# Performance work log

Hardware: AMD Instinct MI355X
Metric: run time of the kernel (lower is better)

The kernel has to match this reference:

```python
import jax, jax.numpy as jnp
import numpy as np

D = 128
EPS = 1e-6


def setup_inputs() -> dict:
    key = jax.random.key(0)
    k1, k2, k3, k4 = jax.random.split(key, 4)
    N, NQ, NK = 32, 2048, 2048
    queries = jax.random.normal(k1, (N, NQ, D), dtype=jnp.float32)
    keys = jax.random.normal(k2, (N, NK, D), dtype=jnp.float32)
    values = jax.random.normal(k3, (N, NK, D), dtype=jnp.float32)
    # multiplicative (soft) mask in [0,1)
    mask = jax.random.uniform(k4, (N, NQ, NK), dtype=jnp.float32)
    return {"queries": queries, "keys": keys, "values": values, "mask": mask}


def reference(queries, keys, values, mask):
    # scaled dot-product scores: N x n_q x n_k
    scaled = jnp.einsum("bqd,bkd->bqk", queries, keys) / jnp.sqrt(jnp.float32(D))
    attn = jax.nn.softmax(scaled, axis=2)
    # post-softmax multiplicative masking + renormalization
    attn = attn * mask
    attn = attn / (jnp.sum(attn, axis=2, keepdims=True) + EPS)
    return jnp.einsum("bqk,bkd->bqd", attn, values)
```

## Files before the change

kernel.cpp:

```cpp
#include <hip/hip_runtime.h>

#define NB   32
#define NQL  2048
#define NKL  2048
#define DH   128
#define QBLK 64
#define KBLK 64
#define NT   (NKL / KBLK)
#define EPS  1e-6f

typedef __bf16 bf16x8 __attribute__((ext_vector_type(8)));
typedef __bf16 bf16x4 __attribute__((ext_vector_type(4)));
typedef float  f32x4  __attribute__((ext_vector_type(4)));

__global__ __launch_bounds__(256) void
prep_k(const float* __restrict__ Kg, unsigned short* __restrict__ Kimg)
{
    const int blk = blockIdx.x;
    const int t   = threadIdx.x;
    const int rK  = t >> 2;
    const int x0  = (t & 3) * 32;
    const int swz = (rK & 7) << 3;
    const float* src = Kg + ((size_t)blk * 64 + rK) * DH;
    unsigned short* dst = Kimg + ((size_t)blk << 13) + rK * 128;
    #pragma unroll
    for (int i = 0; i < 4; ++i) {
        const int c0 = (x0 + i * 8) ^ swz;
        float4 a = *(const float4*)(src + c0);
        float4 c = *(const float4*)(src + c0 + 4);
        *(bf16x8*)(dst + x0 + i * 8) =
            (bf16x8){ (__bf16)a.x, (__bf16)a.y, (__bf16)a.z, (__bf16)a.w,
                      (__bf16)c.x, (__bf16)c.y, (__bf16)c.z, (__bf16)c.w };
    }
}

__global__ __launch_bounds__(256) void
prep_v(const float* __restrict__ Vg, unsigned short* __restrict__ Vimg)
{
    __shared__ float T[64 * 132];
    const int blk = blockIdx.x;
    const int t   = threadIdx.x;
    {
        const int r  = t >> 2;
        const int c0 = (t & 3) * 32;
        const float* src = Vg + ((size_t)blk * 64 + r) * DH + c0;
        #pragma unroll
        for (int j = 0; j < 8; ++j)
            *(float4*)&T[r * 132 + c0 + j * 4] = *(const float4*)(src + j * 4);
    }
    __syncthreads();
    {
        const int dV  = t >> 1;
        const int yh  = (t & 1) * 32;
        const int swz = (dV & 7) << 3;
        unsigned short* dst = Vimg + ((size_t)blk << 13) + dV * 64 + yh;
        #pragma unroll
        for (int i = 0; i < 4; ++i) {
            const int ks = (yh + i * 8) ^ swz;
            bf16x8 o;
            #pragma unroll
            for (int j = 0; j < 8; ++j) o[j] = (__bf16)T[(ks + j) * 132 + dV];
            *(bf16x8*)(dst + i * 8) = o;
        }
    }
}

#define GLL16(GSRC, LDST) \
    __builtin_amdgcn_global_load_lds( \
        (const __attribute__((address_space(1))) void*)(GSRC), \
        (__attribute__((address_space(3))) void*)(LDST), 16, 0, 0)

#define ISSUE_KV(KT, KB, VB) do { \
    const size_t tb_ = ((size_t)(b * 32 + (KT))) << 14;                \
    const char* ksrc_ = (const char*)KimgB + tb_ + woff + lby;                    \
    const char* vsrc_ = (const char*)VimgB + tb_ + woff + lby;                    \
    char* kd_ = (char*)(KB) + woff;                                               \
    char* vd_ = (char*)(VB) + woff;                                               \
    GLL16(ksrc_ +    0, kd_ +    0);  GLL16(ksrc_ + 1024, kd_ + 1024);            \
    GLL16(ksrc_ + 2048, kd_ + 2048);  GLL16(ksrc_ + 3072, kd_ + 3072);            \
    GLL16(vsrc_ +    0, vd_ +    0);  GLL16(vsrc_ + 1024, vd_ + 1024);            \
    GLL16(vsrc_ + 2048, vd_ + 2048);  GLL16(vsrc_ + 3072, vd_ + 3072);            \
} while (0)

#define LOAD_M(K0, R0, R1, R2, R3) do { \
    const float* mb_ = mbase + (K0) + lg * 4; \
    R0 = *(const float4*)(mb_ +  0);  R1 = *(const float4*)(mb_ + 16); \
    R2 = *(const float4*)(mb_ + 32);  R3 = *(const float4*)(mb_ + 48); \
} while (0)

#define COMPUTE(KB, VB, M0, M1, M2, M3) do { \
    f32x4 sacc[4]; \
    _Pragma("unroll") for (int m = 0; m < 4; ++m) sacc[m] = (f32x4){0.f,0.f,0.f,0.f}; \
    __builtin_amdgcn_s_setprio(1); \
    _Pragma("unroll") for (int m = 0; m < 4; ++m) { \
        _Pragma("unroll") for (int c = 0; c < 4; ++c) { \
            bf16x8 af = *(bf16x8*)&KB[(m * 16 + lq) * 128 + ((c * 32 + lg * 8) ^ swzL)]; \
            sacc[m] = __builtin_amdgcn_mfma_f32_16x16x32_bf16(af, qf[c], sacc[m], 0, 0, 0); \
        } \
    } \
    __builtin_amdgcn_s_setprio(0); \
    float mk_[16] = { M0.x, M0.y, M0.z, M0.w,  M1.x, M1.y, M1.z, M1.w, \
                      M2.x, M2.y, M2.z, M2.w,  M3.x, M3.y, M3.z, M3.w }; \
    float sv[4][4], tmax = -1e30f; \
    _Pragma("unroll") for (int m = 0; m < 4; ++m) \
        _Pragma("unroll") for (int r = 0; r < 4; ++r) { \
            sv[m][r] = sacc[m][r] * scale; \
            tmax = fmaxf(tmax, sv[m][r]); \
        } \
    tmax = fmaxf(tmax, __shfl_xor(tmax, 16)); \
    tmax = fmaxf(tmax, __shfl_xor(tmax, 32)); \
    if (!__all(tmax - m_run <= 8.f)) { \
        const float mnew  = fmaxf(m_run, tmax); \
        const float alpha = __expf(m_run - mnew); \
        m_run = mnew;  z_part *= alpha;  s_part *= alpha; \
        float alr[4]; \
        _Pragma("unroll") for (int r = 0; r < 4; ++r) alr[r] = __shfl(alpha, lg * 4 + r); \
        _Pragma("unroll") for (int n = 0; n < 8; ++n) \
            _Pragma("unroll") for (int r = 0; r < 4; ++r) oacc[n][r] *= alr[r]; \
    } \
    float zl = 0.f, sl = 0.f, pm[4][4]; \
    _Pragma("unroll") for (int m = 0; m < 4; ++m) \
        _Pragma("unroll") for (int r = 0; r < 4; ++r) { \
            float p = __expf(sv[m][r] - m_run); \
            zl += p; \
            float pq = p * mk_[m * 4 + r]; \
            sl += pq;  pm[m][r] = pq; \
        } \
    z_part += zl;  s_part += sl; \
    _Pragma("unroll") for (int m = 0; m < 4; ++m) \
        *(bf16x4*)&Ps[w][lq][m * 16 + lg * 4] = \
            (bf16x4){ (__bf16)pm[m][0], (__bf16)pm[m][1], (__bf16)pm[m][2], (__bf16)pm[m][3] }; \
    __builtin_amdgcn_s_setprio(1); \
    _Pragma("unroll") for (int kc = 0; kc < 2; ++kc) { \
        bf16x8 pa = *(bf16x8*)&Ps[w][lq][kc * 32 + lg * 8]; \
        _Pragma("unroll") for (int n = 0; n < 8; ++n) { \
            bf16x8 vv = *(bf16x8*)&VB[(n * 16 + lq) * 64 + ((kc * 32 + lg * 8) ^ swzL)]; \
            oacc[n] = __builtin_amdgcn_mfma_f32_16x16x32_bf16(pa, vv, oacc[n], 0, 0, 0); \
        } \
    } \
    __builtin_amdgcn_s_setprio(0); \
} while (0)

#define ITER(KT, KBc, VBc, KBn, VBn, MU0,MU1,MU2,MU3, ML0,ML1,ML2,ML3, LAST) do { \
    if (!(LAST)) { \
        ISSUE_KV((KT) + 1, KBn, VBn); \
        LOAD_M(((KT) + 1) * KBLK, ML0, ML1, ML2, ML3); \
    } \
    __builtin_amdgcn_sched_barrier(0); \
    COMPUTE(KBc, VBc, MU0, MU1, MU2, MU3); \
    if (!(LAST)) __syncthreads(); \
} while (0)

__global__ __launch_bounds__(256, 2) void
attn_main(const float* __restrict__ Qg, const unsigned short* __restrict__ Kimg,
          const unsigned short* __restrict__ Vimg, const float* __restrict__ Mg,
          float* __restrict__ Og)
{
    const int wg = ((blockIdx.x & 7) << 7) | (blockIdx.x >> 3);
    const int b  = wg >> 5;
    const int q0 = (wg & 31) * QBLK;

    const int t  = threadIdx.x;
    const int w  = t >> 6;
    const int l  = t & 63;
    const int lq = l & 15;
    const int lg = l >> 4;
    const int swzL = (lq & 7) << 3;
    const int woff = w * 4096;
    const int lby  = l * 16;

    __shared__ __align__(16) unsigned short Kb0[64 * 128];
    __shared__ __align__(16) unsigned short Kb1[64 * 128];
    __shared__ __align__(16) unsigned short Vb0[128 * 64];
    __shared__ __align__(16) unsigned short Vb1[128 * 64];
    __shared__ __align__(16) unsigned short Ps[4][16][72];

    const char* KimgB = (const char*)Kimg;
    const char* VimgB = (const char*)Vimg;

    const int qrow = q0 + w * 16 + lq;

    bf16x8 qf[4];
    {
        const float* qb = Qg + ((size_t)b * NQL + qrow) * DH;
        #pragma unroll
        for (int c = 0; c < 4; ++c) {
            const float* p = qb + c * 32 + lg * 8;
            float4 x = *(const float4*)(p);
            float4 y = *(const float4*)(p + 4);
            qf[c] = (bf16x8){ (__bf16)x.x, (__bf16)x.y, (__bf16)x.z, (__bf16)x.w,
                              (__bf16)y.x, (__bf16)y.y, (__bf16)y.z, (__bf16)y.w };
        }
    }

    float m_run = -1e30f, z_part = 0.f, s_part = 0.f;
    f32x4 oacc[8];
    #pragma unroll
    for (int n = 0; n < 8; ++n) oacc[n] = (f32x4){0.f, 0.f, 0.f, 0.f};

    const float* mbase = Mg + ((size_t)b * NQL + qrow) * NKL;
    const float scale = 0.08838834764831845f;

    float4 mA0, mA1, mA2, mA3, mB0, mB1, mB2, mB3;

    ISSUE_KV(0, Kb0, Vb0);
    LOAD_M(0, mA0, mA1, mA2, mA3);
    __syncthreads();

    for (int kt = 0; kt < NT - 2; kt += 2) {
        ITER(kt,     Kb0, Vb0, Kb1, Vb1, mA0,mA1,mA2,mA3, mB0,mB1,mB2,mB3, 0);
        ITER(kt + 1, Kb1, Vb1, Kb0, Vb0, mB0,mB1,mB2,mB3, mA0,mA1,mA2,mA3, 0);
    }
    ITER(NT - 2, Kb0, Vb0, Kb1, Vb1, mA0,mA1,mA2,mA3, mB0,mB1,mB2,mB3, 0);
    ITER(NT - 1, Kb1, Vb1, Kb0, Vb0, mB0,mB1,mB2,mB3, mA0,mA1,mA2,mA3, 1);

    float z = z_part + __shfl_xor(z_part, 16);
    z += __shfl_xor(z, 32);
    float s = s_part + __shfl_xor(s_part, 16);
    s += __shfl_xor(s, 32);
    const float inv = 1.f / (s + EPS * z);
    float ivr[4];
    #pragma unroll
    for (int r = 0; r < 4; ++r) ivr[r] = __shfl(inv, lg * 4 + r);

    float* ob = Og + ((size_t)b * NQL + q0 + w * 16) * DH;
    #pragma unroll
    for (int n = 0; n < 8; ++n)
        #pragma unroll
        for (int r = 0; r < 4; ++r)
            ob[(size_t)(lg * 4 + r) * DH + n * 16 + lq] = oacc[n][r] * ivr[r];
}

__global__ __launch_bounds__(256, 3) void
attn_fb(const float* __restrict__ Qg, const float* __restrict__ Kg,
        const float* __restrict__ Vg, const float* __restrict__ Mg,
        float* __restrict__ Og)
{
    const int wg = ((blockIdx.x & 7) << 7) | (blockIdx.x >> 3);
    const int b  = wg >> 5;
    const int q0 = (wg & 31) * QBLK;
    const int t  = threadIdx.x;
    const int w  = t >> 6;
    const int l  = t & 63;
    const int lq = l & 15;
    const int lg = l >> 4;
    __shared__ __align__(16) unsigned short Ks[64 * 128];
    __shared__ __align__(16) unsigned short Vs[128 * 64];
    __shared__ __align__(16) unsigned short Ps[4][16][72];
    const int rK   = t >> 2;
    const int cK   = (t & 3) * 32;
    const int dV   = t >> 1;
    const int khV  = t & 1;
    const int swzK = (rK & 7) << 3;
    const int swzV = (dV & 7) << 3;
    const int swzL = (lq & 7) << 3;
    const int qrow = q0 + w * 16 + lq;
    bf16x8 qf[4];
    {
        const float* qb = Qg + ((size_t)b * NQL + qrow) * DH;
        #pragma unroll
        for (int c = 0; c < 4; ++c) {
            const float* p = qb + c * 32 + lg * 8;
            float4 x = *(const float4*)(p);
            float4 y = *(const float4*)(p + 4);
            qf[c] = (bf16x8){ (__bf16)x.x, (__bf16)x.y, (__bf16)x.z, (__bf16)x.w,
                              (__bf16)y.x, (__bf16)y.y, (__bf16)y.z, (__bf16)y.w };
        }
    }
    float m_run = -1e30f, z_part = 0.f, s_part = 0.f;
    f32x4 oacc[8];
    #pragma unroll
    for (int n = 0; n < 8; ++n) oacc[n] = (f32x4){0.f, 0.f, 0.f, 0.f};
    const float* kbase = Kg + (size_t)b * NKL * DH;
    const float* vbase = Vg + (size_t)b * NKL * DH;
    const float* mbase = Mg + ((size_t)b * NQL + qrow) * NKL;
    const float scale = 0.08838834764831845f;
    for (int kt = 0; kt < NT; ++kt) {
        const int k0 = kt * KBLK;
        float mkf[16];
        {
            const float* mb = mbase + k0 + lg * 4;
            #pragma unroll
            for (int m = 0; m < 4; ++m) {
                float4 x = *(const float4*)(mb + m * 16);
                mkf[m*4+0]=x.x; mkf[m*4+1]=x.y; mkf[m*4+2]=x.z; mkf[m*4+3]=x.w;
            }
        }
        __syncthreads();
        {
            const float* kb = kbase + (size_t)(k0 + rK) * DH + cK;
            #pragma unroll
            for (int i = 0; i < 4; ++i) {
                float4 a = *(const float4*)(kb + i * 8);
                float4 c = *(const float4*)(kb + i * 8 + 4);
                *(bf16x8*)&Ks[rK * 128 + ((cK + i * 8) ^ swzK)] =
                    (bf16x8){ (__bf16)a.x, (__bf16)a.y, (__bf16)a.z, (__bf16)a.w,
                              (__bf16)c.x, (__bf16)c.y, (__bf16)c.z, (__bf16)c.w };
            }
            const float* vb = vbase + (size_t)(k0 + khV * 32) * DH + dV;
            #pragma unroll
            for (int i = 0; i < 4; ++i) {
                bf16x8 o;
                #pragma unroll
                for (int j = 0; j < 8; ++j) o[j] = (__bf16)vb[(i * 8 + j) * DH];
                *(bf16x8*)&Vs[dV * 64 + (((khV << 5) + i * 8) ^ swzV)] = o;
            }
        }
        __syncthreads();
        f32x4 sacc[4];
        #pragma unroll
        for (int m = 0; m < 4; ++m) sacc[m] = (f32x4){0.f,0.f,0.f,0.f};
        #pragma unroll
        for (int m = 0; m < 4; ++m)
            #pragma unroll
            for (int c = 0; c < 4; ++c) {
                bf16x8 af = *(bf16x8*)&Ks[(m * 16 + lq) * 128 + ((c * 32 + lg * 8) ^ swzL)];
                sacc[m] = __builtin_amdgcn_mfma_f32_16x16x32_bf16(af, qf[c], sacc[m], 0, 0, 0);
            }
        float sv[4][4], tmax = -1e30f;
        #pragma unroll
        for (int m = 0; m < 4; ++m)
            #pragma unroll
            for (int r = 0; r < 4; ++r) {
                sv[m][r] = sacc[m][r] * scale;
                tmax = fmaxf(tmax, sv[m][r]);
            }
        tmax = fmaxf(tmax, __shfl_xor(tmax, 16));
        tmax = fmaxf(tmax, __shfl_xor(tmax, 32));
        if (!__all(tmax - m_run <= 8.f)) {
            const float mnew  = fmaxf(m_run, tmax);
            const float alpha = __expf(m_run - mnew);
            m_run = mnew; z_part *= alpha; s_part *= alpha;
            float alr[4];
            #pragma unroll
            for (int r = 0; r < 4; ++r) alr[r] = __shfl(alpha, lg * 4 + r);
            #pragma unroll
            for (int n = 0; n < 8; ++n)
                #pragma unroll
                for (int r = 0; r < 4; ++r) oacc[n][r] *= alr[r];
        }
        float zl = 0.f, sl = 0.f, pm[4][4];
        #pragma unroll
        for (int m = 0; m < 4; ++m)
            #pragma unroll
            for (int r = 0; r < 4; ++r) {
                float p = __expf(sv[m][r] - m_run);
                zl += p;
                float pq = p * mkf[m * 4 + r];
                sl += pq; pm[m][r] = pq;
            }
        z_part += zl; s_part += sl;
        #pragma unroll
        for (int m = 0; m < 4; ++m)
            *(bf16x4*)&Ps[w][lq][m * 16 + lg * 4] =
                (bf16x4){ (__bf16)pm[m][0], (__bf16)pm[m][1], (__bf16)pm[m][2], (__bf16)pm[m][3] };
        #pragma unroll
        for (int kc = 0; kc < 2; ++kc) {
            bf16x8 pa = *(bf16x8*)&Ps[w][lq][kc * 32 + lg * 8];
            #pragma unroll
            for (int n = 0; n < 8; ++n) {
                bf16x8 vv = *(bf16x8*)&Vs[(n * 16 + lq) * 64 + ((kc * 32 + lg * 8) ^ swzL)];
                oacc[n] = __builtin_amdgcn_mfma_f32_16x16x32_bf16(pa, vv, oacc[n], 0, 0, 0);
            }
        }
    }
    float z = z_part + __shfl_xor(z_part, 16);
    z += __shfl_xor(z, 32);
    float s = s_part + __shfl_xor(s_part, 16);
    s += __shfl_xor(s, 32);
    const float inv = 1.f / (s + EPS * z);
    float ivr[4];
    #pragma unroll
    for (int r = 0; r < 4; ++r) ivr[r] = __shfl(inv, lg * 4 + r);
    float* ob = Og + ((size_t)b * NQL + q0 + w * 16) * DH;
    #pragma unroll
    for (int n = 0; n < 8; ++n)
        #pragma unroll
        for (int r = 0; r < 4; ++r)
            ob[(size_t)(lg * 4 + r) * DH + n * 16 + lq] = oacc[n][r] * ivr[r];
}

extern "C" void kernel_launch(void* const* d_in, const int* in_sizes, int n_in,
                              void* d_out, int out_size, void* d_ws, size_t ws_size,
                              hipStream_t stream)
{
    (void)in_sizes; (void)n_in; (void)out_size;
    const float* Q = (const float*)d_in[0];
    const float* K = (const float*)d_in[1];
    const float* V = (const float*)d_in[2];
    const float* M = (const float*)d_in[3];
    float* O = (float*)d_out;

    const size_t imgElems = (size_t)NB * NKL * DH;
    const size_t need     = 2 * imgElems * sizeof(unsigned short);

    if (ws_size >= need) {
        unsigned short* Kimg = (unsigned short*)d_ws;
        unsigned short* Vimg = Kimg + imgElems;
        prep_k<<<dim3(NB * NT), 256, 0, stream>>>(K, Kimg);
        prep_v<<<dim3(NB * NT), 256, 0, stream>>>(V, Vimg);
        attn_main<<<dim3(NB * (NQL / QBLK)), 256, 0, stream>>>(Q, Kimg, Vimg, M, O);
    } else {
        attn_fb<<<dim3(NB * (NQL / QBLK)), 256, 0, stream>>>(Q, K, V, M, O);
    }
}
```

Baseline: 195.3 us.

## Stage K/V tiles through registers two tiles ahead and merge prep kernels

Replaces the direct global-to-LDS async loads with register-staged loads that fetch tile kt+2 into VGPRs while tile kt computes, then write them to LDS at the start of the next iteration. The full __syncthreads is replaced by an lgkmcnt wait plus s_barrier, so outstanding global loads (the prefetched tile and mask) no longer have to drain at each barrier. The K and V prep kernels are merged into a single launch. The cost is extra VGPR pressure under launch_bounds(256,2) and extra LDS write instructions. The code relies on KimgB/VimgB being char pointers, which is set up in lines not shown.

```diff
diff --git a/kernel.cpp b/kernel.cpp
--- a/kernel.cpp
+++ b/kernel.cpp
@@ -14,72 +14,72 @@
 typedef float  f32x4  __attribute__((ext_vector_type(4)));
 
 __global__ __launch_bounds__(256) void
-prep_k(const float* __restrict__ Kg, unsigned short* __restrict__ Kimg)
-{
-    const int blk = blockIdx.x;
-    const int t   = threadIdx.x;
-    const int rK  = t >> 2;
-    const int x0  = (t & 3) * 32;
-    const int swz = (rK & 7) << 3;
-    const float* src = Kg + ((size_t)blk * 64 + rK) * DH;
-    unsigned short* dst = Kimg + ((size_t)blk << 13) + rK * 128;
-    #pragma unroll
-    for (int i = 0; i < 4; ++i) {
-        const int c0 = (x0 + i * 8) ^ swz;
-        float4 a = *(const float4*)(src + c0);
-        float4 c = *(const float4*)(src + c0 + 4);
-        *(bf16x8*)(dst + x0 + i * 8) =
-            (bf16x8){ (__bf16)a.x, (__bf16)a.y, (__bf16)a.z, (__bf16)a.w,
-                      (__bf16)c.x, (__bf16)c.y, (__bf16)c.z, (__bf16)c.w };
-    }
-}
-
-__global__ __launch_bounds__(256) void
-prep_v(const float* __restrict__ Vg, unsigned short* __restrict__ Vimg)
+prep_kv(const float* __restrict__ Kg, const float* __restrict__ Vg,
+        unsigned short* __restrict__ Kimg, unsigned short* __restrict__ Vimg)
 {
     __shared__ float T[64 * 132];
-    const int blk = blockIdx.x;
-    const int t   = threadIdx.x;
-    {
-        const int r  = t >> 2;
-        const int c0 = (t & 3) * 32;
-        const float* src = Vg + ((size_t)blk * 64 + r) * DH + c0;
-        #pragma unroll
-        for (int j = 0; j < 8; ++j)
-            *(float4*)&T[r * 132 + c0 + j * 4] = *(const float4*)(src + j * 4);
-    }
-    __syncthreads();
-    {
-        const int dV  = t >> 1;
-        const int yh  = (t & 1) * 32;
-        const int swz = (dV & 7) << 3;
-        unsigned short* dst = Vimg + ((size_t)blk << 13) + dV * 64 + yh;
+    const int t = threadIdx.x;
+    if (blockIdx.x < NB * NT) {
+        const int blk = blockIdx.x;
+        const int rK  = t >> 2;
+        const int x0  = (t & 3) * 32;
+        const int swz = (rK & 7) << 3;
+        const float* src = Kg + ((size_t)blk * 64 + rK) * DH;
+        unsigned short* dst = Kimg + ((size_t)blk << 13) + rK * 128;
         #pragma unroll
         for (int i = 0; i < 4; ++i) {
-            const int ks = (yh + i * 8) ^ swz;
-            bf16x8 o;
-            #pragma unroll
-            for (int j = 0; j < 8; ++j) o[j] = (__bf16)T[(ks + j) * 132 + dV];
-            *(bf16x8*)(dst + i * 8) = o;
+            const int c0 = (x0 + i * 8) ^ swz;
+            float4 a = *(const float4*)(src + c0);
+            float4 c = *(const float4*)(src + c0 + 4);
+            *(bf16x8*)(dst + x0 + i * 8) =
+                (bf16x8){ (__bf16)a.x, (__bf16)a.y, (__bf16)a.z, (__bf16)a.w,
+                          (__bf16)c.x, (__bf16)c.y, (__bf16)c.z, (__bf16)c.w };
+        }
+    } else {
+        const int blk = blockIdx.x - NB * NT;
+        {
+            const int r  = t >> 2;
+            const int c0 = (t & 3) * 32;
+            const float* src = Vg + ((size_t)blk * 64 + r) * DH + c0;
+            #pragma unroll
+            for (int j = 0; j < 8; ++j)
+                *(float4*)&T[r * 132 + c0 + j * 4] = *(const float4*)(src + j * 4);
+        }
+        __syncthreads();
+        {
+            const int dV  = t >> 1;
+            const int yh  = (t & 1) * 32;
+            const int swz = (dV & 7) << 3;
+            unsigned short* dst = Vimg + ((size_t)blk << 13) + dV * 64 + yh;
+            #pragma unroll
+            for (int i = 0; i < 4; ++i) {
+                const int ks = (yh + i * 8) ^ swz;
+                bf16x8 o;
+                #pragma unroll
+                for (int j = 0; j < 8; ++j) o[j] = (__bf16)T[(ks + j) * 132 + dV];
+                *(bf16x8*)(dst + i * 8) = o;
+            }
         }
     }
 }
 
-#define GLL16(GSRC, LDST) \
-    __builtin_amdgcn_global_load_lds( \
-        (const __attribute__((address_space(1))) void*)(GSRC), \
-        (__attribute__((address_space(3))) void*)(LDST), 16, 0, 0)
-
-#define ISSUE_KV(KT, KB, VB) do { \
-    const size_t tb_ = ((size_t)(b * 32 + (KT))) << 14;                \
-    const char* ksrc_ = (const char*)KimgB + tb_ + woff + lby;                    \
-    const char* vsrc_ = (const char*)VimgB + tb_ + woff + lby;                    \
-    char* kd_ = (char*)(KB) + woff;                                               \
-    char* vd_ = (char*)(VB) + woff;                                               \
-    GLL16(ksrc_ +    0, kd_ +    0);  GLL16(ksrc_ + 1024, kd_ + 1024);            \
-    GLL16(ksrc_ + 2048, kd_ + 2048);  GLL16(ksrc_ + 3072, kd_ + 3072);            \
-    GLL16(vsrc_ +    0, vd_ +    0);  GLL16(vsrc_ + 1024, vd_ + 1024);            \
-    GLL16(vsrc_ + 2048, vd_ + 2048);  GLL16(vsrc_ + 3072, vd_ + 3072);            \
+
+#define LOAD_IMG(KT) do { \
+    const char* ks_ = KimgB + (((size_t)(b * 32 + (KT))) << 14) + woff + lby; \
+    const char* vs_ = VimgB + (((size_t)(b * 32 + (KT))) << 14) + woff + lby; \
+    ik0 = *(const bf16x8*)(ks_ +    0);  ik1 = *(const bf16x8*)(ks_ + 1024); \
+    ik2 = *(const bf16x8*)(ks_ + 2048);  ik3 = *(const bf16x8*)(ks_ + 3072); \
+    iv0 = *(const bf16x8*)(vs_ +    0);  iv1 = *(const bf16x8*)(vs_ + 1024); \
+    iv2 = *(const bf16x8*)(vs_ + 2048);  iv3 = *(const bf16x8*)(vs_ + 3072); \
+} while (0)
+
+#define STW_IMG(KB, VB) do { \
+    char* kd_ = (char*)(KB) + woff + lby; \
+    char* vd_ = (char*)(VB) + woff + lby; \
+    *(bf16x8*)(kd_ +    0) = ik0;  *(bf16x8*)(kd_ + 1024) = ik1; \
+    *(bf16x8*)(kd_ + 2048) = ik2;  *(bf16x8*)(kd_ + 3072) = ik3; \
+    *(bf16x8*)(vd_ +    0) = iv0;  *(bf16x8*)(vd_ + 1024) = iv1; \
+    *(bf16x8*)(vd_ + 2048) = iv2;  *(bf16x8*)(vd_ + 3072) = iv3; \
 } while (0)
 
 #define LOAD_M(K0, R0, R1, R2, R3) do { \
@@ -141,14 +141,19 @@
     __builtin_amdgcn_s_setprio(0); \
 } while (0)
 
-#define ITER(KT, KBc, VBc, KBn, VBn, MU0,MU1,MU2,MU3, ML0,ML1,ML2,ML3, LAST) do { \
-    if (!(LAST)) { \
-        ISSUE_KV((KT) + 1, KBn, VBn); \
-        LOAD_M(((KT) + 1) * KBLK, ML0, ML1, ML2, ML3); \
-    } \
+#define SOFT_BARRIER() do { \
+    asm volatile("s_waitcnt lgkmcnt(0)" ::: "memory"); \
     __builtin_amdgcn_sched_barrier(0); \
+    __builtin_amdgcn_s_barrier(); \
+    __builtin_amdgcn_sched_barrier(0); \
+} while (0)
+
+#define ITER(KT, KBc, VBc, KBn, VBn, MU0,MU1,MU2,MU3, ML0,ML1,ML2,ML3) do { \
+    if ((KT) + 1 < NT) STW_IMG(KBn, VBn); \
+    if ((KT) + 2 < NT) LOAD_IMG((KT) + 2); \
+    if ((KT) + 1 < NT) LOAD_M(((KT) + 1) * KBLK, ML0, ML1, ML2, ML3); \
     COMPUTE(KBc, VBc, MU0, MU1, MU2, MU3); \
-    if (!(LAST)) __syncthreads(); \
+    if ((KT) + 1 < NT) SOFT_BARRIER(); \
 } while (0)
 
 __global__ __launch_bounds__(256, 2) void
@@ -201,18 +206,19 @@
     const float* mbase = Mg + ((size_t)b * NQL + qrow) * NKL;
     const float scale = 0.08838834764831845f;
 
+    bf16x8 ik0, ik1, ik2, ik3, iv0, iv1, iv2, iv3;
     float4 mA0, mA1, mA2, mA3, mB0, mB1, mB2, mB3;
 
-    ISSUE_KV(0, Kb0, Vb0);
+    LOAD_IMG(0);
     LOAD_M(0, mA0, mA1, mA2, mA3);
-    __syncthreads();
-
-    for (int kt = 0; kt < NT - 2; kt += 2) {
-        ITER(kt,     Kb0, Vb0, Kb1, Vb1, mA0,mA1,mA2,mA3, mB0,mB1,mB2,mB3, 0);
-        ITER(kt + 1, Kb1, Vb1, Kb0, Vb0, mB0,mB1,mB2,mB3, mA0,mA1,mA2,mA3, 0);
-    }
-    ITER(NT - 2, Kb0, Vb0, Kb1, Vb1, mA0,mA1,mA2,mA3, mB0,mB1,mB2,mB3, 0);
-    ITER(NT - 1, Kb1, Vb1, Kb0, Vb0, mB0,mB1,mB2,mB3, mA0,mA1,mA2,mA3, 1);
+    STW_IMG(Kb0, Vb0);
+    LOAD_IMG(1);
+    SOFT_BARRIER();
+
+    for (int kt = 0; kt < NT; kt += 2) {
+        ITER(kt,     Kb0, Vb0, Kb1, Vb1, mA0,mA1,mA2,mA3, mB0,mB1,mB2,mB3);
+        ITER(kt + 1, Kb1, Vb1, Kb0, Vb0, mB0,mB1,mB2,mB3, mA0,mA1,mA2,mA3);
+    }
 
     float z = z_part + __shfl_xor(z_part, 16);
     z += __shfl_xor(z, 32);
@@ -397,8 +403,7 @@
     if (ws_size >= need) {
         unsigned short* Kimg = (unsigned short*)d_ws;
         unsigned short* Vimg = Kimg + imgElems;
-        prep_k<<<dim3(NB * NT), 256, 0, stream>>>(K, Kimg);
-        prep_v<<<dim3(NB * NT), 256, 0, stream>>>(V, Vimg);
+        prep_kv<<<dim3(2 * NB * NT), 256, 0, stream>>>(K, V, Kimg, Vimg);
         attn_main<<<dim3(NB * (NQL / QBLK)), 256, 0, stream>>>(Q, Kimg, Vimg, M, O);
     } else {
         attn_fb<<<dim3(NB * (NQL / QBLK)), 256, 0, stream>>>(Q, K, V, M, O);
```

Measured after the change: 193.7 us. About the same (-0.8%).

## Double query tile per workgroup to reuse K/V tiles and merge prep kernels

Applied to the files above, without the earlier changes.

The query block grows from 64 to 128 rows, so each wave now handles two 16-row query halves. Each K fragment read from LDS feeds two QK MFMAs, and each staged K/V tile is shared by twice as many queries. This halves global K/V image traffic and the number of LDS fills. The K and V bf16 prep kernels are merged into a single launch to save one kernel launch. In exchange, each wave keeps two sets of accumulators and mask registers, which raises register pressure, and there are half as many workgroups to fill the GPU.

```diff
diff --git a/kernel.cpp b/kernel.cpp
--- a/kernel.cpp
+++ b/kernel.cpp
@@ -4,7 +4,7 @@
 #define NQL  2048
 #define NKL  2048
 #define DH   128
-#define QBLK 64
+#define QBLK 128
 #define KBLK 64
 #define NT   (NKL / KBLK)
 #define EPS  1e-6f
@@ -14,119 +14,111 @@
 typedef float  f32x4  __attribute__((ext_vector_type(4)));
 
 __global__ __launch_bounds__(256) void
-prep_k(const float* __restrict__ Kg, unsigned short* __restrict__ Kimg)
-{
-    const int blk = blockIdx.x;
-    const int t   = threadIdx.x;
-    const int rK  = t >> 2;
-    const int x0  = (t & 3) * 32;
-    const int swz = (rK & 7) << 3;
-    const float* src = Kg + ((size_t)blk * 64 + rK) * DH;
-    unsigned short* dst = Kimg + ((size_t)blk << 13) + rK * 128;
-    #pragma unroll
-    for (int i = 0; i < 4; ++i) {
-        const int c0 = (x0 + i * 8) ^ swz;
-        float4 a = *(const float4*)(src + c0);
-        float4 c = *(const float4*)(src + c0 + 4);
-        *(bf16x8*)(dst + x0 + i * 8) =
-            (bf16x8){ (__bf16)a.x, (__bf16)a.y, (__bf16)a.z, (__bf16)a.w,
-                      (__bf16)c.x, (__bf16)c.y, (__bf16)c.z, (__bf16)c.w };
-    }
-}
-
-__global__ __launch_bounds__(256) void
-prep_v(const float* __restrict__ Vg, unsigned short* __restrict__ Vimg)
+prep_kv(const float* __restrict__ Kg, const float* __restrict__ Vg,
+        unsigned short* __restrict__ Kimg, unsigned short* __restrict__ Vimg)
 {
     __shared__ float T[64 * 132];
-    const int blk = blockIdx.x;
-    const int t   = threadIdx.x;
-    {
-        const int r  = t >> 2;
-        const int c0 = (t & 3) * 32;
-        const float* src = Vg + ((size_t)blk * 64 + r) * DH + c0;
-        #pragma unroll
-        for (int j = 0; j < 8; ++j)
-            *(float4*)&T[r * 132 + c0 + j * 4] = *(const float4*)(src + j * 4);
-    }
-    __syncthreads();
-    {
-        const int dV  = t >> 1;
-        const int yh  = (t & 1) * 32;
-        const int swz = (dV & 7) << 3;
-        unsigned short* dst = Vimg + ((size_t)blk << 13) + dV * 64 + yh;
+    const int t = threadIdx.x;
+    if (blockIdx.x < NB * NT) {
+        const int blk = blockIdx.x;
+        const int rK  = t >> 2;
+        const int x0  = (t & 3) * 32;
+        const int swz = (rK & 7) << 3;
+        const float* src = Kg + ((size_t)blk * 64 + rK) * DH;
+        unsigned short* dst = Kimg + ((size_t)blk << 13) + rK * 128;
         #pragma unroll
         for (int i = 0; i < 4; ++i) {
-            const int ks = (yh + i * 8) ^ swz;
-            bf16x8 o;
-            #pragma unroll
-            for (int j = 0; j < 8; ++j) o[j] = (__bf16)T[(ks + j) * 132 + dV];
-            *(bf16x8*)(dst + i * 8) = o;
+            const int c0 = (x0 + i * 8) ^ swz;
+            float4 a = *(const float4*)(src + c0);
+            float4 c = *(const float4*)(src + c0 + 4);
+            *(bf16x8*)(dst + x0 + i * 8) =
+                (bf16x8){ (__bf16)a.x, (__bf16)a.y, (__bf16)a.z, (__bf16)a.w,
+                          (__bf16)c.x, (__bf16)c.y, (__bf16)c.z, (__bf16)c.w };
+        }
+    } else {
+        const int blk = blockIdx.x - NB * NT;
+        {
+            const int r  = t >> 2;
+            const int c0 = (t & 3) * 32;
+            const float* src = Vg + ((size_t)blk * 64 + r) * DH + c0;
+            #pragma unroll
+            for (int j = 0; j < 8; ++j)
+                *(float4*)&T[r * 132 + c0 + j * 4] = *(const float4*)(src + j * 4);
+        }
+        __syncthreads();
+        {
+            const int dV  = t >> 1;
+            const int yh  = (t & 1) * 32;
+            const int swz = (dV & 7) << 3;
+            unsigned short* dst = Vimg + ((size_t)blk << 13) + dV * 64 + yh;
+            #pragma unroll
+            for (int i = 0; i < 4; ++i) {
+                const int ks = (yh + i * 8) ^ swz;
+                bf16x8 o;
+                #pragma unroll
+                for (int j = 0; j < 8; ++j) o[j] = (__bf16)T[(ks + j) * 132 + dV];
+                *(bf16x8*)(dst + i * 8) = o;
+            }
         }
     }
 }
+
 
 #define GLL16(GSRC, LDST) \
     __builtin_amdgcn_global_load_lds( \
         (const __attribute__((address_space(1))) void*)(GSRC), \
         (__attribute__((address_space(3))) void*)(LDST), 16, 0, 0)
 
-#define ISSUE_KV(KT, KB, VB) do { \
-    const size_t tb_ = ((size_t)(b * 32 + (KT))) << 14;                \
-    const char* ksrc_ = (const char*)KimgB + tb_ + woff + lby;                    \
-    const char* vsrc_ = (const char*)VimgB + tb_ + woff + lby;                    \
-    char* kd_ = (char*)(KB) + woff;                                               \
-    char* vd_ = (char*)(VB) + woff;                                               \
-    GLL16(ksrc_ +    0, kd_ +    0);  GLL16(ksrc_ + 1024, kd_ + 1024);            \
-    GLL16(ksrc_ + 2048, kd_ + 2048);  GLL16(ksrc_ + 3072, kd_ + 3072);            \
-    GLL16(vsrc_ +    0, vd_ +    0);  GLL16(vsrc_ + 1024, vd_ + 1024);            \
-    GLL16(vsrc_ + 2048, vd_ + 2048);  GLL16(vsrc_ + 3072, vd_ + 3072);            \
+#define ISSUE_KV(KT, KB_, VB_) do { \
+    const size_t tb_ = ((size_t)(b * 32 + (KT))) << 14; \
+    const char* ksrc_ = KimgB + tb_ + woff + lby; \
+    const char* vsrc_ = VimgB + tb_ + woff + lby; \
+    char* kd_ = (char*)(KB_) + woff; \
+    char* vd_ = (char*)(VB_) + woff; \
+    GLL16(ksrc_ +    0, kd_ +    0);  GLL16(ksrc_ + 1024, kd_ + 1024); \
+    GLL16(ksrc_ + 2048, kd_ + 2048);  GLL16(ksrc_ + 3072, kd_ + 3072); \
+    GLL16(vsrc_ +    0, vd_ +    0);  GLL16(vsrc_ + 1024, vd_ + 1024); \
+    GLL16(vsrc_ + 2048, vd_ + 2048);  GLL16(vsrc_ + 3072, vd_ + 3072); \
 } while (0)
 
-#define LOAD_M(K0, R0, R1, R2, R3) do { \
-    const float* mb_ = mbase + (K0) + lg * 4; \
-    R0 = *(const float4*)(mb_ +  0);  R1 = *(const float4*)(mb_ + 16); \
-    R2 = *(const float4*)(mb_ + 32);  R3 = *(const float4*)(mb_ + 48); \
+#define LOAD_M2(K0, R0,R1,R2,R3,R4,R5,R6,R7) do { \
+    const float* ma_ = mbase0 + (K0); \
+    const float* mc_ = mbase1 + (K0); \
+    R0 = *(const float4*)(ma_ +  0);  R1 = *(const float4*)(ma_ + 16); \
+    R2 = *(const float4*)(ma_ + 32);  R3 = *(const float4*)(ma_ + 48); \
+    R4 = *(const float4*)(mc_ +  0);  R5 = *(const float4*)(mc_ + 16); \
+    R6 = *(const float4*)(mc_ + 32);  R7 = *(const float4*)(mc_ + 48); \
 } while (0)
 
-#define COMPUTE(KB, VB, M0, M1, M2, M3) do { \
-    f32x4 sacc[4]; \
-    _Pragma("unroll") for (int m = 0; m < 4; ++m) sacc[m] = (f32x4){0.f,0.f,0.f,0.f}; \
-    __builtin_amdgcn_s_setprio(1); \
-    _Pragma("unroll") for (int m = 0; m < 4; ++m) { \
-        _Pragma("unroll") for (int c = 0; c < 4; ++c) { \
-            bf16x8 af = *(bf16x8*)&KB[(m * 16 + lq) * 128 + ((c * 32 + lg * 8) ^ swzL)]; \
-            sacc[m] = __builtin_amdgcn_mfma_f32_16x16x32_bf16(af, qf[c], sacc[m], 0, 0, 0); \
-        } \
-    } \
-    __builtin_amdgcn_s_setprio(0); \
+#define HALF_TAIL(SA, M0, M1, M2, M3, MRUN, ZP, SP, OA, VB) do { \
     float mk_[16] = { M0.x, M0.y, M0.z, M0.w,  M1.x, M1.y, M1.z, M1.w, \
                       M2.x, M2.y, M2.z, M2.w,  M3.x, M3.y, M3.z, M3.w }; \
     float sv[4][4], tmax = -1e30f; \
     _Pragma("unroll") for (int m = 0; m < 4; ++m) \
         _Pragma("unroll") for (int r = 0; r < 4; ++r) { \
-            sv[m][r] = sacc[m][r] * scale; \
+            sv[m][r] = SA[m][r] * scale; \
             tmax = fmaxf(tmax, sv[m][r]); \
         } \
     tmax = fmaxf(tmax, __shfl_xor(tmax, 16)); \
     tmax = fmaxf(tmax, __shfl_xor(tmax, 32)); \
-    if (!__all(tmax - m_run <= 8.f)) { \
-        const float mnew  = fmaxf(m_run, tmax); \
-        const float alpha = __expf(m_run - mnew); \
-        m_run = mnew;  z_part *= alpha;  s_part *= alpha; \
+    if (!__all(tmax - MRUN <= 8.f)) { \
+        const float mnew_  = fmaxf(MRUN, tmax); \
+        const float alpha_ = __expf(MRUN - mnew_); \
+        MRUN = mnew_;  ZP *= alpha_;  SP *= alpha_; \
         float alr[4]; \
-        _Pragma("unroll") for (int r = 0; r < 4; ++r) alr[r] = __shfl(alpha, lg * 4 + r); \
+        _Pragma("unroll") for (int r = 0; r < 4; ++r) alr[r] = __shfl(alpha_, lg * 4 + r); \
         _Pragma("unroll") for (int n = 0; n < 8; ++n) \
-            _Pragma("unroll") for (int r = 0; r < 4; ++r) oacc[n][r] *= alr[r]; \
+            _Pragma("unroll") for (int r = 0; r < 4; ++r) OA[n][r] *= alr[r]; \
     } \
     float zl = 0.f, sl = 0.f, pm[4][4]; \
     _Pragma("unroll") for (int m = 0; m < 4; ++m) \
         _Pragma("unroll") for (int r = 0; r < 4; ++r) { \
-            float p = __expf(sv[m][r] - m_run); \
+            float p = __expf(sv[m][r] - MRUN); \
             zl += p; \
             float pq = p * mk_[m * 4 + r]; \
             sl += pq;  pm[m][r] = pq; \
         } \
-    z_part += zl;  s_part += sl; \
+    ZP += zl;  SP += sl; \
     _Pragma("unroll") for (int m = 0; m < 4; ++m) \
         *(bf16x4*)&Ps[w][lq][m * 16 + lg * 4] = \
             (bf16x4){ (__bf16)pm[m][0], (__bf16)pm[m][1], (__bf16)pm[m][2], (__bf16)pm[m][3] }; \
@@ -135,19 +127,39 @@
         bf16x8 pa = *(bf16x8*)&Ps[w][lq][kc * 32 + lg * 8]; \
         _Pragma("unroll") for (int n = 0; n < 8; ++n) { \
             bf16x8 vv = *(bf16x8*)&VB[(n * 16 + lq) * 64 + ((kc * 32 + lg * 8) ^ swzL)]; \
-            oacc[n] = __builtin_amdgcn_mfma_f32_16x16x32_bf16(pa, vv, oacc[n], 0, 0, 0); \
+            OA[n] = __builtin_amdgcn_mfma_f32_16x16x32_bf16(pa, vv, OA[n], 0, 0, 0); \
         } \
     } \
     __builtin_amdgcn_s_setprio(0); \
 } while (0)
 
-#define ITER(KT, KBc, VBc, KBn, VBn, MU0,MU1,MU2,MU3, ML0,ML1,ML2,ML3, LAST) do { \
+#define COMPUTE(KB, VB, M0,M1,M2,M3,M4,M5,M6,M7) do { \
+    f32x4 sa0[4], sa1[4]; \
+    _Pragma("unroll") for (int m = 0; m < 4; ++m) { \
+        sa0[m] = (f32x4){0.f,0.f,0.f,0.f};  sa1[m] = (f32x4){0.f,0.f,0.f,0.f}; \
+    } \
+    __builtin_amdgcn_s_setprio(1); \
+    _Pragma("unroll") for (int m = 0; m < 4; ++m) { \
+        _Pragma("unroll") for (int c = 0; c < 4; ++c) { \
+            bf16x8 af = *(bf16x8*)&KB[(m * 16 + lq) * 128 + ((c * 32 + lg * 8) ^ swzL)]; \
+            sa0[m] = __builtin_amdgcn_mfma_f32_16x16x32_bf16(af, qf0[c], sa0[m], 0, 0, 0); \
+            sa1[m] = __builtin_amdgcn_mfma_f32_16x16x32_bf16(af, qf1[c], sa1[m], 0, 0, 0); \
+        } \
+    } \
+    __builtin_amdgcn_s_setprio(0); \
+    HALF_TAIL(sa0, M0,M1,M2,M3, m_run0, z0, s0, oacc0, VB); \
+    HALF_TAIL(sa1, M4,M5,M6,M7, m_run1, z1, s1, oacc1, VB); \
+} while (0)
+
+#define ITER(KT, KBc, VBc, KBn, VBn, \
+             MU0,MU1,MU2,MU3,MU4,MU5,MU6,MU7, \
+             ML0,ML1,ML2,ML3,ML4,ML5,ML6,ML7, LAST) do { \
     if (!(LAST)) { \
         ISSUE_KV((KT) + 1, KBn, VBn); \
-        LOAD_M(((KT) + 1) * KBLK, ML0, ML1, ML2, ML3); \
+        LOAD_M2(((KT) + 1) * KBLK, ML0,ML1,ML2,ML3,ML4,ML5,ML6,ML7); \
     } \
     __builtin_amdgcn_sched_barrier(0); \
-    COMPUTE(KBc, VBc, MU0, MU1, MU2, MU3); \
+    COMPUTE(KBc, VBc, MU0,MU1,MU2,MU3,MU4,MU5,MU6,MU7); \
     if (!(LAST)) __syncthreads(); \
 } while (0)
 
@@ -156,9 +168,9 @@
           const unsigned short* __restrict__ Vimg, const float* __restrict__ Mg,
           float* __restrict__ Og)
 {
-    const int wg = ((blockIdx.x & 7) << 7) | (blockIdx.x >> 3);
-    const int b  = wg >> 5;
-    const int q0 = (wg & 31) * QBLK;
+    const int wg = ((blockIdx.x & 7) << 6) | (blockIdx.x >> 3);
+    const int b  = wg >> 4;
+    const int qt = wg & 15;
 
     const int t  = threadIdx.x;
     const int w  = t >> 6;
@@ -178,57 +190,90 @@
     const char* KimgB = (const char*)Kimg;
     const char* VimgB = (const char*)Vimg;
 
-    const int qrow = q0 + w * 16 + lq;
-
-    bf16x8 qf[4];
+    const int qbase = qt * QBLK + w * 32;
+    const int qrow0 = qbase + lq;
+    const int qrow1 = qbase + 16 + lq;
+
+    bf16x8 qf0[4], qf1[4];
     {
-        const float* qb = Qg + ((size_t)b * NQL + qrow) * DH;
+        const float* qb0 = Qg + ((size_t)b * NQL + qrow0) * DH;
+        const float* qb1 = Qg + ((size_t)b * NQL + qrow1) * DH;
         #pragma unroll
         for (int c = 0; c < 4; ++c) {
-            const float* p = qb + c * 32 + lg * 8;
-            float4 x = *(const float4*)(p);
-            float4 y = *(const float4*)(p + 4);
-            qf[c] = (bf16x8){ (__bf16)x.x, (__bf16)x.y, (__bf16)x.z, (__bf16)x.w,
-                              (__bf16)y.x, (__bf16)y.y, (__bf16)y.z, (__bf16)y.w };
-        }
-    }
-
-    float m_run = -1e30f, z_part = 0.f, s_part = 0.f;
-    f32x4 oacc[8];
+            const float* p0 = qb0 + c * 32 + lg * 8;
+            const float* p1 = qb1 + c * 32 + lg * 8;
+            float4 x0 = *(const float4*)(p0), y0 = *(const float4*)(p0 + 4);
+            float4 x1 = *(const float4*)(p1), y1 = *(const float4*)(p1 + 4);
+            qf0[c] = (bf16x8){ (__bf16)x0.x, (__bf16)x0.y, (__bf16)x0.z, (__bf16)x0.w,
+                               (__bf16)y0.x, (__bf16)y0.y, (__bf16)y0.z, (__bf16)y0.w };
+            qf1[c] = (bf16x8){ (__bf16)x1.x, (__bf16)x1.y, (__bf16)x1.z, (__bf16)x1.w,
+                               (__bf16)y1.x, (__bf16)y1.y, (__bf16)y1.z, (__bf16)y1.w };
+        }
+    }
+
+    float m_run0 = -1e30f, z0 = 0.f, s0 = 0.f;
+    float m_run1 = -1e30f, z1 = 0.f, s1 = 0.f;
+    f32x4 oacc0[8], oacc1[8];
     #pragma unroll
-    for (int n = 0; n < 8; ++n) oacc[n] = (f32x4){0.f, 0.f, 0.f, 0.f};
-
-    const float* mbase = Mg + ((size_t)b * NQL + qrow) * NKL;
+    for (int n = 0; n < 8; ++n) {
+        oacc0[n] = (f32x4){0.f, 0.f, 0.f, 0.f};
+        oacc1[n] = (f32x4){0.f, 0.f, 0.f, 0.f};
+    }
+
+    const float* mbase0 = Mg + ((size_t)b * NQL + qrow0) * NKL + lg * 4;
+    const float* mbase1 = Mg + ((size_t)b * NQL + qrow1) * NKL + lg * 4;
     const float scale = 0.08838834764831845f;
 
-    float4 mA0, mA1, mA2, mA3, mB0, mB1, mB2, mB3;
+    float4 mA0, mA1, mA2, mA3, mA4, mA5, mA6, mA7;
+    float4 mB0, mB1, mB2, mB3, mB4, mB5, mB6, mB7;
 
     ISSUE_KV(0, Kb0, Vb0);
-    LOAD_M(0, mA0, mA1, mA2, mA3);
+    LOAD_M2(0, mA0,mA1,mA2,mA3,mA4,mA5,mA6,mA7);
     __syncthreads();
 
     for (int kt = 0; kt < NT - 2; kt += 2) {
-        ITER(kt,     Kb0, Vb0, Kb1, Vb1, mA0,mA1,mA2,mA3, mB0,mB1,mB2,mB3, 0);
-        ITER(kt + 1, Kb1, Vb1, Kb0, Vb0, mB0,mB1,mB2,mB3, mA0,mA1,mA2,mA3, 0);
-    }
-    ITER(NT - 2, Kb0, Vb0, Kb1, Vb1, mA0,mA1,mA2,mA3, mB0,mB1,mB2,mB3, 0);
-    ITER(NT - 1, Kb1, Vb1, Kb0, Vb0, mB0,mB1,mB2,mB3, mA0,mA1,mA2,mA3, 1);
-
-    float z = z_part + __shfl_xor(z_part, 16);
-    z += __shfl_xor(z, 32);
-    float s = s_part + __shfl_xor(s_part, 16);
-    s += __shfl_xor(s, 32);
-    const float inv = 1.f / (s + EPS * z);
-    float ivr[4];
-    #pragma unroll
-    for (int r = 0; r < 4; ++r) ivr[r] = __shfl(inv, lg * 4 + r);
-
-    float* ob = Og + ((size_t)b * NQL + q0 + w * 16) * DH;
-    #pragma unroll
-    for (int n = 0; n < 8; ++n)
-        #pragma unroll
-        for (int r = 0; r < 4; ++r)
-            ob[(size_t)(lg * 4 + r) * DH + n * 16 + lq] = oacc[n][r] * ivr[r];
+        ITER(kt,     Kb0, Vb0, Kb1, Vb1,
+             mA0,mA1,mA2,mA3,mA4,mA5,mA6,mA7,
+             mB0,mB1,mB2,mB3,mB4,mB5,mB6,mB7, 0);
+        ITER(kt + 1, Kb1, Vb1, Kb0, Vb0,
+             mB0,mB1,mB2,mB3,mB4,mB5,mB6,mB7,
+             mA0,mA1,mA2,mA3,mA4,mA5,mA6,mA7, 0);
+    }
+    ITER(NT - 2, Kb0, Vb0, Kb1, Vb1,
+         mA0,mA1,mA2,mA3,mA4,mA5,mA6,mA7,
+         mB0,mB1,mB2,mB3,mB4,mB5,mB6,mB7, 0);
+    ITER(NT - 1, Kb1, Vb1, Kb0, Vb0,
+         mB0,mB1,mB2,mB3,mB4,mB5,mB6,mB7,
+         mA0,mA1,mA2,mA3,mA4,mA5,mA6,mA7, 1);
+
+    {
+        float z = z0 + __shfl_xor(z0, 16);  z += __shfl_xor(z, 32);
+        float s = s0 + __shfl_xor(s0, 16);  s += __shfl_xor(s, 32);
+        const float inv = 1.f / (s + EPS * z);
+        float ivr[4];
+        #pragma unroll
+        for (int r = 0; r < 4; ++r) ivr[r] = __shfl(inv, lg * 4 + r);
+        float* ob = Og + ((size_t)b * NQL + qbase) * DH;
+        #pragma unroll
+        for (int n = 0; n < 8; ++n)
+            #pragma unroll
+            for (int r = 0; r < 4; ++r)
+                ob[(size_t)(lg * 4 + r) * DH + n * 16 + lq] = oacc0[n][r] * ivr[r];
+    }
+    {
+        float z = z1 + __shfl_xor(z1, 16);  z += __shfl_xor(z, 32);
+        float s = s1 + __shfl_xor(s1, 16);  s += __shfl_xor(s, 32);
+        const float inv = 1.f / (s + EPS * z);
+        float ivr[4];
+        #pragma unroll
+        for (int r = 0; r < 4; ++r) ivr[r] = __shfl(inv, lg * 4 + r);
+        float* ob = Og + ((size_t)b * NQL + qbase + 16) * DH;
+        #pragma unroll
+        for (int n = 0; n < 8; ++n)
+            #pragma unroll
+            for (int r = 0; r < 4; ++r)
+                ob[(size_t)(lg * 4 + r) * DH + n * 16 + lq] = oacc1[n][r] * ivr[r];
+    }
 }
 
 __global__ __launch_bounds__(256, 3) void
@@ -238,7 +283,7 @@
 {
     const int wg = ((blockIdx.x & 7) << 7) | (blockIdx.x >> 3);
     const int b  = wg >> 5;
-    const int q0 = (wg & 31) * QBLK;
+    const int q0 = (wg & 31) * 64;
     const int t  = threadIdx.x;
     const int w  = t >> 6;
     const int l  = t & 63;
@@ -397,10 +442,9 @@
     if (ws_size >= need) {
         unsigned short* Kimg = (unsigned short*)d_ws;
         unsigned short* Vimg = Kimg + imgElems;
-        prep_k<<<dim3(NB * NT), 256, 0, stream>>>(K, Kimg);
-        prep_v<<<dim3(NB * NT), 256, 0, stream>>>(V, Vimg);
+        prep_kv<<<dim3(2 * NB * NT), 256, 0, stream>>>(K, V, Kimg, Vimg);
         attn_main<<<dim3(NB * (NQL / QBLK)), 256, 0, stream>>>(Q, Kimg, Vimg, M, O);
     } else {
-        attn_fb<<<dim3(NB * (NQL / QBLK)), 256, 0, stream>>>(Q, K, V, M, O);
+        attn_fb<<<dim3(NB * (NQL / 64)), 256, 0, stream>>>(Q, K, V, M, O);
     }
 }
```

Result: slower. 269.5 us (+38.0%).

## Double query tile to 128 with 512-thread blocks and merge K/V prep kernels

Applied to the files above, without the earlier changes.

Each workgroup now covers 128 query rows with 8 waves, so every K/V tile staged in LDS serves twice as many queries, and each thread issues half as many async global-to-LDS loads. The P staging buffer shrinks to a 32-column half-tile that is written and read per kc step, cutting LDS use so more blocks can fit. The K and V conversion kernels are merged into one launch to save a kernel launch. In exchange there are fewer workgroups (512), a larger block, and an extra LDS round trip per kc half, which adds latency and may lower occupancy.

```diff
diff --git a/kernel.cpp b/kernel.cpp
--- a/kernel.cpp
+++ b/kernel.cpp
@@ -4,7 +4,7 @@
 #define NQL  2048
 #define NKL  2048
 #define DH   128
-#define QBLK 64
+#define QBLK 128
 #define KBLK 64
 #define NT   (NKL / KBLK)
 #define EPS  1e-6f
@@ -14,76 +14,73 @@
 typedef float  f32x4  __attribute__((ext_vector_type(4)));
 
 __global__ __launch_bounds__(256) void
-prep_k(const float* __restrict__ Kg, unsigned short* __restrict__ Kimg)
-{
-    const int blk = blockIdx.x;
-    const int t   = threadIdx.x;
-    const int rK  = t >> 2;
-    const int x0  = (t & 3) * 32;
-    const int swz = (rK & 7) << 3;
-    const float* src = Kg + ((size_t)blk * 64 + rK) * DH;
-    unsigned short* dst = Kimg + ((size_t)blk << 13) + rK * 128;
-    #pragma unroll
-    for (int i = 0; i < 4; ++i) {
-        const int c0 = (x0 + i * 8) ^ swz;
-        float4 a = *(const float4*)(src + c0);
-        float4 c = *(const float4*)(src + c0 + 4);
-        *(bf16x8*)(dst + x0 + i * 8) =
-            (bf16x8){ (__bf16)a.x, (__bf16)a.y, (__bf16)a.z, (__bf16)a.w,
-                      (__bf16)c.x, (__bf16)c.y, (__bf16)c.z, (__bf16)c.w };
-    }
-}
-
-__global__ __launch_bounds__(256) void
-prep_v(const float* __restrict__ Vg, unsigned short* __restrict__ Vimg)
+prep_kv(const float* __restrict__ Kg, const float* __restrict__ Vg,
+        unsigned short* __restrict__ Kimg, unsigned short* __restrict__ Vimg)
 {
     __shared__ float T[64 * 132];
-    const int blk = blockIdx.x;
-    const int t   = threadIdx.x;
-    {
-        const int r  = t >> 2;
-        const int c0 = (t & 3) * 32;
-        const float* src = Vg + ((size_t)blk * 64 + r) * DH + c0;
-        #pragma unroll
-        for (int j = 0; j < 8; ++j)
-            *(float4*)&T[r * 132 + c0 + j * 4] = *(const float4*)(src + j * 4);
-    }
-    __syncthreads();
-    {
-        const int dV  = t >> 1;
-        const int yh  = (t & 1) * 32;
-        const int swz = (dV & 7) << 3;
-        unsigned short* dst = Vimg + ((size_t)blk << 13) + dV * 64 + yh;
+    const int t = threadIdx.x;
+    if (blockIdx.x < NB * NT) {
+        const int blk = blockIdx.x;
+        const int rK  = t >> 2;
+        const int x0  = (t & 3) * 32;
+        const int swz = (rK & 7) << 3;
+        const float* src = Kg + ((size_t)blk * 64 + rK) * DH;
+        unsigned short* dst = Kimg + ((size_t)blk << 13) + rK * 128;
         #pragma unroll
         for (int i = 0; i < 4; ++i) {
-            const int ks = (yh + i * 8) ^ swz;
-            bf16x8 o;
-            #pragma unroll
-            for (int j = 0; j < 8; ++j) o[j] = (__bf16)T[(ks + j) * 132 + dV];
-            *(bf16x8*)(dst + i * 8) = o;
+            const int c0 = (x0 + i * 8) ^ swz;
+            float4 a = *(const float4*)(src + c0);
+            float4 c = *(const float4*)(src + c0 + 4);
+            *(bf16x8*)(dst + x0 + i * 8) =
+                (bf16x8){ (__bf16)a.x, (__bf16)a.y, (__bf16)a.z, (__bf16)a.w,
+                          (__bf16)c.x, (__bf16)c.y, (__bf16)c.z, (__bf16)c.w };
+        }
+    } else {
+        const int blk = blockIdx.x - NB * NT;
+        {
+            const int r  = t >> 2;
+            const int c0 = (t & 3) * 32;
+            const float* src = Vg + ((size_t)blk * 64 + r) * DH + c0;
+            #pragma unroll
+            for (int j = 0; j < 8; ++j)
+                *(float4*)&T[r * 132 + c0 + j * 4] = *(const float4*)(src + j * 4);
+        }
+        __syncthreads();
+        {
+            const int dV  = t >> 1;
+            const int yh  = (t & 1) * 32;
+            const int swz = (dV & 7) << 3;
+            unsigned short* dst = Vimg + ((size_t)blk << 13) + dV * 64 + yh;
+            #pragma unroll
+            for (int i = 0; i < 4; ++i) {
+                const int ks = (yh + i * 8) ^ swz;
+                bf16x8 o;
+                #pragma unroll
+                for (int j = 0; j < 8; ++j) o[j] = (__bf16)T[(ks + j) * 132 + dV];
+                *(bf16x8*)(dst + i * 8) = o;
+            }
         }
     }
 }
+
 
 #define GLL16(GSRC, LDST) \
     __builtin_amdgcn_global_load_lds( \
         (const __attribute__((address_space(1))) void*)(GSRC), \
         (__attribute__((address_space(3))) void*)(LDST), 16, 0, 0)
 
-#define ISSUE_KV(KT, KB, VB) do { \
-    const size_t tb_ = ((size_t)(b * 32 + (KT))) << 14;                \
-    const char* ksrc_ = (const char*)KimgB + tb_ + woff + lby;                    \
-    const char* vsrc_ = (const char*)VimgB + tb_ + woff + lby;                    \
-    char* kd_ = (char*)(KB) + woff;                                               \
-    char* vd_ = (char*)(VB) + woff;                                               \
-    GLL16(ksrc_ +    0, kd_ +    0);  GLL16(ksrc_ + 1024, kd_ + 1024);            \
-    GLL16(ksrc_ + 2048, kd_ + 2048);  GLL16(ksrc_ + 3072, kd_ + 3072);            \
-    GLL16(vsrc_ +    0, vd_ +    0);  GLL16(vsrc_ + 1024, vd_ + 1024);            \
-    GLL16(vsrc_ + 2048, vd_ + 2048);  GLL16(vsrc_ + 3072, vd_ + 3072);            \
+#define ISSUE_KV(KT, KB_, VB_) do { \
+    const size_t tb_ = ((size_t)(b * 32 + (KT))) << 14; \
+    const char* ksrc_ = KimgB + tb_ + woff + lby; \
+    const char* vsrc_ = VimgB + tb_ + woff + lby; \
+    char* kd_ = (char*)(KB_) + woff; \
+    char* vd_ = (char*)(VB_) + woff; \
+    GLL16(ksrc_ +    0, kd_ +    0);  GLL16(ksrc_ + 1024, kd_ + 1024); \
+    GLL16(vsrc_ +    0, vd_ +    0);  GLL16(vsrc_ + 1024, vd_ + 1024); \
 } while (0)
 
 #define LOAD_M(K0, R0, R1, R2, R3) do { \
-    const float* mb_ = mbase + (K0) + lg * 4; \
+    const float* mb_ = mbase + (K0); \
     R0 = *(const float4*)(mb_ +  0);  R1 = *(const float4*)(mb_ + 16); \
     R2 = *(const float4*)(mb_ + 32);  R3 = *(const float4*)(mb_ + 48); \
 } while (0)
@@ -110,11 +107,11 @@
     tmax = fmaxf(tmax, __shfl_xor(tmax, 16)); \
     tmax = fmaxf(tmax, __shfl_xor(tmax, 32)); \
     if (!__all(tmax - m_run <= 8.f)) { \
-        const float mnew  = fmaxf(m_run, tmax); \
-        const float alpha = __expf(m_run - mnew); \
-        m_run = mnew;  z_part *= alpha;  s_part *= alpha; \
+        const float mnew_  = fmaxf(m_run, tmax); \
+        const float alpha_ = __expf(m_run - mnew_); \
+        m_run = mnew_;  z_part *= alpha_;  s_part *= alpha_; \
         float alr[4]; \
-        _Pragma("unroll") for (int r = 0; r < 4; ++r) alr[r] = __shfl(alpha, lg * 4 + r); \
+        _Pragma("unroll") for (int r = 0; r < 4; ++r) alr[r] = __shfl(alpha_, lg * 4 + r); \
         _Pragma("unroll") for (int n = 0; n < 8; ++n) \
             _Pragma("unroll") for (int r = 0; r < 4; ++r) oacc[n][r] *= alr[r]; \
     } \
@@ -127,18 +124,21 @@
             sl += pq;  pm[m][r] = pq; \
         } \
     z_part += zl;  s_part += sl; \
-    _Pragma("unroll") for (int m = 0; m < 4; ++m) \
-        *(bf16x4*)&Ps[w][lq][m * 16 + lg * 4] = \
-            (bf16x4){ (__bf16)pm[m][0], (__bf16)pm[m][1], (__bf16)pm[m][2], (__bf16)pm[m][3] }; \
-    __builtin_amdgcn_s_setprio(1); \
     _Pragma("unroll") for (int kc = 0; kc < 2; ++kc) { \
-        bf16x8 pa = *(bf16x8*)&Ps[w][lq][kc * 32 + lg * 8]; \
+        *(bf16x4*)&Ps[w][lq][lg * 4] = \
+            (bf16x4){ (__bf16)pm[2*kc][0], (__bf16)pm[2*kc][1], \
+                      (__bf16)pm[2*kc][2], (__bf16)pm[2*kc][3] }; \
+        *(bf16x4*)&Ps[w][lq][16 + lg * 4] = \
+            (bf16x4){ (__bf16)pm[2*kc+1][0], (__bf16)pm[2*kc+1][1], \
+                      (__bf16)pm[2*kc+1][2], (__bf16)pm[2*kc+1][3] }; \
+        bf16x8 pa = *(bf16x8*)&Ps[w][lq][lg * 8]; \
+        __builtin_amdgcn_s_setprio(1); \
         _Pragma("unroll") for (int n = 0; n < 8; ++n) { \
             bf16x8 vv = *(bf16x8*)&VB[(n * 16 + lq) * 64 + ((kc * 32 + lg * 8) ^ swzL)]; \
             oacc[n] = __builtin_amdgcn_mfma_f32_16x16x32_bf16(pa, vv, oacc[n], 0, 0, 0); \
         } \
+        __builtin_amdgcn_s_setprio(0); \
     } \
-    __builtin_amdgcn_s_setprio(0); \
 } while (0)
 
 #define ITER(KT, KBc, VBc, KBn, VBn, MU0,MU1,MU2,MU3, ML0,ML1,ML2,ML3, LAST) do { \
@@ -151,14 +151,14 @@
     if (!(LAST)) __syncthreads(); \
 } while (0)
 
-__global__ __launch_bounds__(256, 2) void
+__global__ __launch_bounds__(512, 4) void
 attn_main(const float* __restrict__ Qg, const unsigned short* __restrict__ Kimg,
           const unsigned short* __restrict__ Vimg, const float* __restrict__ Mg,
           float* __restrict__ Og)
 {
-    const int wg = ((blockIdx.x & 7) << 7) | (blockIdx.x >> 3);
-    const int b  = wg >> 5;
-    const int q0 = (wg & 31) * QBLK;
+    const int wg = ((blockIdx.x & 7) << 6) | (blockIdx.x >> 3);
+    const int b  = wg >> 4;
+    const int qt = wg & 15;
 
     const int t  = threadIdx.x;
     const int w  = t >> 6;
@@ -166,19 +166,19 @@
     const int lq = l & 15;
     const int lg = l >> 4;
     const int swzL = (lq & 7) << 3;
-    const int woff = w * 4096;
+    const int woff = w * 2048;
     const int lby  = l * 16;
 
     __shared__ __align__(16) unsigned short Kb0[64 * 128];
     __shared__ __align__(16) unsigned short Kb1[64 * 128];
     __shared__ __align__(16) unsigned short Vb0[128 * 64];
     __shared__ __align__(16) unsigned short Vb1[128 * 64];
-    __shared__ __align__(16) unsigned short Ps[4][16][72];
+    __shared__ __align__(16) unsigned short Ps[8][16][40];
 
     const char* KimgB = (const char*)Kimg;
     const char* VimgB = (const char*)Vimg;
 
-    const int qrow = q0 + w * 16 + lq;
+    const int qrow = qt * QBLK + w * 16 + lq;
 
     bf16x8 qf[4];
     {
@@ -198,7 +198,7 @@
     #pragma unroll
     for (int n = 0; n < 8; ++n) oacc[n] = (f32x4){0.f, 0.f, 0.f, 0.f};
 
-    const float* mbase = Mg + ((size_t)b * NQL + qrow) * NKL;
+    const float* mbase = Mg + ((size_t)b * NQL + qrow) * NKL + lg * 4;
     const float scale = 0.08838834764831845f;
 
     float4 mA0, mA1, mA2, mA3, mB0, mB1, mB2, mB3;
@@ -223,7 +223,7 @@
     #pragma unroll
     for (int r = 0; r < 4; ++r) ivr[r] = __shfl(inv, lg * 4 + r);
 
-    float* ob = Og + ((size_t)b * NQL + q0 + w * 16) * DH;
+    float* ob = Og + ((size_t)b * NQL + qt * QBLK + w * 16) * DH;
     #pragma unroll
     for (int n = 0; n < 8; ++n)
         #pragma unroll
@@ -238,7 +238,7 @@
 {
     const int wg = ((blockIdx.x & 7) << 7) | (blockIdx.x >> 3);
     const int b  = wg >> 5;
-    const int q0 = (wg & 31) * QBLK;
+    const int q0 = (wg & 31) * 64;
     const int t  = threadIdx.x;
     const int w  = t >> 6;
     const int l  = t & 63;
@@ -397,10 +397,9 @@
     if (ws_size >= need) {
         unsigned short* Kimg = (unsigned short*)d_ws;
         unsigned short* Vimg = Kimg + imgElems;
-        prep_k<<<dim3(NB * NT), 256, 0, stream>>>(K, Kimg);
-        prep_v<<<dim3(NB * NT), 256, 0, stream>>>(V, Vimg);
-        attn_main<<<dim3(NB * (NQL / QBLK)), 256, 0, stream>>>(Q, Kimg, Vimg, M, O);
+        prep_kv<<<dim3(2 * NB * NT), 256, 0, stream>>>(K, V, Kimg, Vimg);
+        attn_main<<<dim3(NB * (NQL / QBLK)), 512, 0, stream>>>(Q, Kimg, Vimg, M, O);
     } else {
-        attn_fb<<<dim3(NB * (NQL / QBLK)), 256, 0, stream>>>(Q, K, V, M, O);
+        attn_fb<<<dim3(NB * (NQL / 64)), 256, 0, stream>>>(Q, K, V, M, O);
     }
 }
```

Result: slower. 241.0 us (+23.4%).
